# Kernel tuning notes

Measured on AMD Instinct MI355X. Metric: run time of the kernel, lower is better.

## Reference

```python
import jax, jax.numpy as jnp
import numpy as np

N_NODES = 10000
N_EDGES = 100000
IN_CH = 384
PROJ = 768  # in_channels * projection_factor
N_BLOCKS = 4
OUT_CH = 128
LN_EPS = 1e-5


def _p(key, shape, fan_in):
    return jax.random.normal(key, shape, dtype=jnp.float32) * (1.0 / np.sqrt(fan_in))


def setup_inputs() -> dict:
    key = jax.random.key(0)
    ks = iter(jax.random.split(key, 64))
    x = jax.random.normal(next(ks), (N_NODES, IN_CH), dtype=jnp.float32)
    edge_index = jax.random.randint(next(ks), (2, N_EDGES), 0, N_NODES, dtype=jnp.int64)
    inp = {
        'x': x,
        'edge_index': edge_index,
        'proj_W': _p(next(ks), (PROJ, IN_CH), IN_CH),
        'proj_b': jnp.zeros((PROJ,), jnp.float32),
        'norm_w': jnp.ones((N_BLOCKS, PROJ), jnp.float32),
        'norm_b': jnp.zeros((N_BLOCKS, PROJ), jnp.float32),
        'g1_W': _p(next(ks), (N_BLOCKS, 4 * 192, PROJ), PROJ),
        'g1_as': _p(next(ks), (N_BLOCKS, 4, 192), 192),
        'g1_ad': _p(next(ks), (N_BLOCKS, 4, 192), 192),
        'g1_b': jnp.zeros((N_BLOCKS, 4 * 192), jnp.float32),
        'g2_W': _p(next(ks), (N_BLOCKS, 2 * 96, PROJ), PROJ),
        'g2_as': _p(next(ks), (N_BLOCKS, 2, 96), 96),
        'g2_ad': _p(next(ks), (N_BLOCKS, 2, 96), 96),
        'g2_b': jnp.zeros((N_BLOCKS, 2 * 96), jnp.float32),
        'uni_W': _p(next(ks), (N_BLOCKS, PROJ, 960), 960),
        'uni_b': jnp.zeros((N_BLOCKS, PROJ), jnp.float32),
        'fnorm_w': jnp.ones((PROJ,), jnp.float32),
        'fnorm_b': jnp.zeros((PROJ,), jnp.float32),
        'fg_W': _p(next(ks), (8 * OUT_CH, PROJ), PROJ),
        'fg_as': _p(next(ks), (8, OUT_CH), OUT_CH),
        'fg_ad': _p(next(ks), (8, OUT_CH), OUT_CH),
        'fg_b': jnp.zeros((OUT_CH,), jnp.float32),
    }
    return inp


def layer_norm(x, w, b):
    m = x.mean(-1, keepdims=True)
    v = ((x - m) ** 2).mean(-1, keepdims=True)
    return (x - m) / jnp.sqrt(v + LN_EPS) * w + b


def gat_conv(x, src, dst, W, a_src, a_dst, bias, heads, out_ch, concat):
    # PyG GATConv (eval mode, add_self_loops already applied in src/dst).
    n = x.shape[0]
    h = (x @ W.T).reshape(n, heads, out_ch)          # [N,H,C]
    al_s = jnp.einsum('nhc,hc->nh', h, a_src)        # [N,H]
    al_d = jnp.einsum('nhc,hc->nh', h, a_dst)
    e = jax.nn.leaky_relu(al_s[src] + al_d[dst], 0.2)  # [E,H]
    emax = jax.ops.segment_max(e, dst, num_segments=n)
    ee = jnp.exp(e - emax[dst])
    den = jax.ops.segment_sum(ee, dst, num_segments=n)
    alpha = ee / (den[dst] + 1e-16)                  # softmax over incoming edges
    out = jax.ops.segment_sum(h[src] * alpha[:, :, None], dst, num_segments=n)
    out = out.reshape(n, heads * out_ch) if concat else out.mean(axis=1)
    return out + bias


def reference(x, edge_index, proj_W, proj_b, norm_w, norm_b,
              g1_W, g1_as, g1_ad, g1_b, g2_W, g2_as, g2_ad, g2_b,
              uni_W, uni_b, fnorm_w, fnorm_b, fg_W, fg_as, fg_ad, fg_b):
    n = x.shape[0]
    loop = jnp.arange(n, dtype=edge_index.dtype)
    src = jnp.concatenate([edge_index[0], loop])  # add self loops (PyG default)
    dst = jnp.concatenate([edge_index[1], loop])

    h = jax.nn.elu(x @ proj_W.T + proj_b)
    for i in range(N_BLOCKS):
        res = h
        hn = layer_norm(h, norm_w[i], norm_b[i])
        o1 = gat_conv(hn, src, dst, g1_W[i], g1_as[i], g1_ad[i], g1_b[i], 4, 192, True)
        o2 = gat_conv(hn, src, dst, g2_W[i], g2_as[i], g2_ad[i], g2_b[i], 2, 96, True)
        cat = jax.nn.elu(jnp.concatenate([o1, o2], axis=-1))  # [N,960]
        h = jax.nn.elu(res + cat @ uni_W[i].T + uni_b[i])
    h = layer_norm(h, fnorm_w, fnorm_b)
    return gat_conv(h, src, dst, fg_W, fg_as, fg_ad, fg_b, 8, OUT_CH, False)
```

## Files before the change

### kernel.cpp

```cpp
#include <hip/hip_runtime.h>
#include <math.h>

#define N_NODES 10000
#define N_EDGES 100000
#define E_TOT   (N_EDGES + N_NODES)
#define PROJ    768
#define LN_EPS  1e-5f

typedef __attribute__((ext_vector_type(8))) short bf16x8;
typedef __attribute__((ext_vector_type(4))) short bf16x4;
typedef __attribute__((ext_vector_type(4))) float f32x4;

__device__ __forceinline__ float elu_f(float x){ return x > 0.f ? x : __expf(x) - 1.f; }
__device__ __forceinline__ float bf2f(unsigned short u){ return __uint_as_float(((unsigned int)u) << 16); }
__device__ __forceinline__ unsigned short f2bf(float f){
  unsigned int u = __float_as_uint(f);
  return (unsigned short)((u + 0x7FFFu + ((u >> 16) & 1u)) >> 16);
}

#define GLOAD16(gp, lp) __builtin_amdgcn_global_load_lds((const __attribute__((address_space(1))) void*)(gp), (__attribute__((address_space(3))) void*)(lp), 16, 0, 0)

__global__ void k_count(const int* __restrict__ ei, int* __restrict__ cnt){
  int e = blockIdx.x*blockDim.x + threadIdx.x;
  if (e >= E_TOT) return;
  int dst = (e < N_EDGES) ? ei[N_EDGES + e] : (e - N_EDGES);
  atomicAdd(&cnt[dst], 1);
}

__global__ void k_scan(const int* __restrict__ cnt, int* __restrict__ indptr){
  __shared__ int s[1024];
  __shared__ int s_running;
  int t = threadIdx.x;
  if (t == 0) s_running = 0;
  __syncthreads();
  for (int base = 0; base < N_NODES; base += 1024){
    int v = (base + t < N_NODES) ? cnt[base + t] : 0;
    s[t] = v; __syncthreads();
    for (int off = 1; off < 1024; off <<= 1){
      int add = (t >= off) ? s[t - off] : 0;
      __syncthreads();
      s[t] += add;
      __syncthreads();
    }
    int total = s[1023];
    int run = s_running;
    if (base + t < N_NODES) indptr[base + t] = run + s[t] - v;
    __syncthreads();
    if (t == 0) s_running = run + total;
    __syncthreads();
  }
  if (t == 0) indptr[N_NODES] = s_running;
}

__global__ void k_copy_int(const int* __restrict__ src, int* __restrict__ dst, int n){
  int i = blockIdx.x*blockDim.x + threadIdx.x;
  if (i < n) dst[i] = src[i];
}

__global__ void k_fill(const int* __restrict__ ei, int* __restrict__ pos,
                       int* __restrict__ csr_src, int* __restrict__ csr_dst){
  int e = blockIdx.x*blockDim.x + threadIdx.x;
  if (e >= E_TOT) return;
  int s, d;
  if (e < N_EDGES){ s = ei[e]; d = ei[N_EDGES + e]; }
  else            { s = d = e - N_EDGES; }
  int p = atomicAdd(&pos[d], 1);
  csr_src[p] = s;
  csr_dst[p] = d;
}

__global__ void k_f2bf_arr4(const float4* __restrict__ in, ushort4* __restrict__ out, int n4){
  int i = blockIdx.x*blockDim.x + threadIdx.x;
  if (i < n4){
    float4 v = in[i];
    ushort4 o;
    o.x = f2bf(v.x); o.y = f2bf(v.y); o.z = f2bf(v.z); o.w = f2bf(v.w);
    out[i] = o;
  }
}

__global__ void k_pack_l1l2(const float* __restrict__ g1, const float* __restrict__ g2,
                            unsigned short* __restrict__ dst){
  int i = blockIdx.x*blockDim.x + threadIdx.x;
  if (i >= 737280) return;
  int layer = i / 184320;
  int off4  = i - layer*184320;
  float4 v;
  if (off4 < 147456) v = *((const float4*)(g1 + (size_t)layer*589824) + off4);
  else               v = *((const float4*)(g2 + (size_t)layer*147456) + (off4 - 147456));
  ushort4 o;
  o.x = f2bf(v.x); o.y = f2bf(v.y); o.z = f2bf(v.z); o.w = f2bf(v.w);
  ((ushort4*)(dst + (size_t)layer*737280))[off4] = o;
}

__global__ void k_layernorm_bf(const unsigned short* __restrict__ x, const float* __restrict__ w,
                               const float* __restrict__ b, unsigned short* __restrict__ y){
  int n = blockIdx.x;
  int t = threadIdx.x;
  const unsigned short* xr = x + (size_t)n*PROJ;
  float v0=0.f, v1=0.f, v2=0.f, v3=0.f;
  if (t < 192){
    bf16x4 hv = *(const bf16x4*)(xr + t*4);
    v0 = bf2f((unsigned short)hv.x); v1 = bf2f((unsigned short)hv.y);
    v2 = bf2f((unsigned short)hv.z); v3 = bf2f((unsigned short)hv.w);
  }
  float s  = v0+v1+v2+v3;
  float s2 = v0*v0 + v1*v1 + v2*v2 + v3*v3;
  #pragma unroll
  for (int off = 32; off; off >>= 1){ s += __shfl_down(s, off); s2 += __shfl_down(s2, off); }
  __shared__ float rs[4], rs2[4];
  __shared__ float s_mean, s_rstd;
  int wid = t >> 6, lane = t & 63;
  if (lane == 0){ rs[wid] = s; rs2[wid] = s2; }
  __syncthreads();
  if (t == 0){
    float S  = rs[0]+rs[1]+rs[2]+rs[3];
    float S2 = rs2[0]+rs2[1]+rs2[2]+rs2[3];
    float m  = S * (1.f/768.f);
    float var = S2 * (1.f/768.f) - m*m;
    s_mean = m; s_rstd = rsqrtf(var + LN_EPS);
  }
  __syncthreads();
  if (t < 192){
    float m = s_mean, r = s_rstd;
    float4 wv = *(const float4*)&w[t*4];
    float4 bv = *(const float4*)&b[t*4];
    ushort4 o;
    o.x = f2bf((v0-m)*r*wv.x + bv.x);
    o.y = f2bf((v1-m)*r*wv.y + bv.y);
    o.z = f2bf((v2-m)*r*wv.z + bv.z);
    o.w = f2bf((v3-m)*r*wv.w + bv.w);
    *(ushort4*)(y + (size_t)n*PROJ + t*4) = o;
  }
}

template<int EPI>
__global__ __launch_bounds__(256, 8)
void k_gemm_mfma(const unsigned short* __restrict__ A, int lda,
                 const unsigned short* __restrict__ W,
                 unsigned short* __restrict__ C, int ldc,
                 int M, int N, int K,
                 const float* __restrict__ bias,
                 const unsigned short* __restrict__ res, int ldres, int NBN){
  __shared__ unsigned short As[2][128*32];
  __shared__ unsigned short Bs[2][64*32];
  const int tid = threadIdx.x;
  const int lane = tid & 63, wid = tid >> 6;
  const int wm = wid >> 1, wn = wid & 1;

  const int nwg = gridDim.x;
  const int q = nwg >> 3, r = nwg & 7;
  const int xcd = blockIdx.x & 7, o = blockIdx.x >> 3;
  const int swz = (xcd < r ? xcd*(q+1) : r*(q+1) + (xcd - r)*q) + o;
  const int bm = (swz / NBN) * 128;
  const int bn = (swz % NBN) * 64;

  const int srow = tid >> 2;
  const int sc   = (tid & 3) ^ ((tid >> 3) & 3);
  size_t ga0 = (size_t)min(bm + srow,      M-1)*lda + sc*8;
  size_t ga1 = (size_t)min(bm + 64 + srow, M-1)*lda + sc*8;
  size_t gb0 = (size_t)min(bn + srow,      N-1)*K   + sc*8;
  const int ldst = tid*8;

  f32x4 acc[4][2];
  #pragma unroll
  for (int i=0;i<4;i++)
    #pragma unroll
    for (int j=0;j<2;j++) acc[i][j] = (f32x4){0.f,0.f,0.f,0.f};

  const int rA = wm*64 + (lane & 15);
  const int rB = wn*32 + (lane & 15);
  const int cu = (((lane >> 4)) ^ (((lane & 15) >> 1) & 3)) * 8;

  const int NT = K >> 5;
  int cur = 0;
  GLOAD16(A + ga0, &As[0][ldst]);
  GLOAD16(A + ga1, &As[0][2048 + ldst]);
  GLOAD16(W + gb0, &Bs[0][ldst]);

  for (int t = 0; t < NT; ++t){
    if (t + 1 < NT){
      const int k0 = (t+1) << 5;
      GLOAD16(A + ga0 + k0, &As[cur^1][ldst]);
      GLOAD16(A + ga1 + k0, &As[cur^1][2048 + ldst]);
      GLOAD16(W + gb0 + k0, &Bs[cur^1][ldst]);
      asm volatile("s_waitcnt vmcnt(3)" ::: "memory");
    } else {
      asm volatile("s_waitcnt vmcnt(0)" ::: "memory");
    }
    __builtin_amdgcn_sched_barrier(0);
    __builtin_amdgcn_s_barrier();
    __builtin_amdgcn_sched_barrier(0);

    bf16x8 af[4], bfr[2];
    #pragma unroll
    for (int mi = 0; mi < 4; mi++)
      af[mi] = *(const bf16x8*)&As[cur][(rA + mi*16)*32 + cu];
    #pragma unroll
    for (int ni = 0; ni < 2; ni++)
      bfr[ni] = *(const bf16x8*)&Bs[cur][(rB + ni*16)*32 + cu];
    #pragma unroll
    for (int mi = 0; mi < 4; mi++)
      #pragma unroll
      for (int ni = 0; ni < 2; ni++)
        acc[mi][ni] = __builtin_amdgcn_mfma_f32_16x16x32_bf16(af[mi], bfr[ni], acc[mi][ni], 0,0,0);

    asm volatile("s_waitcnt lgkmcnt(0)" ::: "memory");
    __builtin_amdgcn_sched_barrier(0);
    __builtin_amdgcn_s_barrier();
    __builtin_amdgcn_sched_barrier(0);
    cur ^= 1;
  }

  const int mrow0 = bm + wm*64 + ((lane>>4)<<2);
  const int ncol0 = bn + wn*32 + (lane & 15);
  #pragma unroll
  for (int mi=0; mi<4; mi++){
    #pragma unroll
    for (int rr=0; rr<4; rr++){
      int m = mrow0 + mi*16 + rr;
      if (m >= M) continue;
      #pragma unroll
      for (int ni=0; ni<2; ni++){
        int n = ncol0 + ni*16;
        float v = acc[mi][ni][rr];
        if (EPI == 1){
          v = elu_f(v + bias[n]);
        } else if (EPI == 2){
          v = elu_f(v + bias[n] + bf2f(res[(size_t)m*ldres + n]));
        }
        C[(size_t)m*ldc + n] = f2bf(v);
      }
    }
  }
}

__global__ void k_attn_coef6(const unsigned short* __restrict__ hlin,
                             const float* __restrict__ as1, const float* __restrict__ ad1,
                             const float* __restrict__ as2, const float* __restrict__ ad2,
                             float* __restrict__ als, float* __restrict__ ald){
  int n = blockIdx.x;
  int wid = threadIdx.x >> 6, lane = threadIdx.x & 63;
  int C    = wid < 4 ? 192 : 96;
  int base = wid < 4 ? wid*192 : 768 + (wid-4)*96;
  const float* as_ = wid < 4 ? as1 + wid*192 : as2 + (wid-4)*96;
  const float* ad_ = wid < 4 ? ad1 + wid*192 : ad2 + (wid-4)*96;
  float ss = 0.f, sd = 0.f;
  if (lane*4 < C){
    bf16x4 hv = *(const bf16x4*)(hlin + (size_t)n*960 + base + lane*4);
    float4 a1 = *(const float4*)&as_[lane*4];
    float4 a2 = *(const float4*)&ad_[lane*4];
    float h0 = bf2f((unsigned short)hv.x), h1 = bf2f((unsigned short)hv.y);
    float h2 = bf2f((unsigned short)hv.z), h3 = bf2f((unsigned short)hv.w);
    ss = h0*a1.x + h1*a1.y + h2*a1.z + h3*a1.w;
    sd = h0*a2.x + h1*a2.y + h2*a2.z + h3*a2.w;
  }
  #pragma unroll
  for (int off = 32; off; off >>= 1){ ss += __shfl_down(ss, off); sd += __shfl_down(sd, off); }
  if (lane == 0){ als[n*6 + wid] = ss; ald[n*6 + wid] = sd; }
}

__global__ void k_attn_coef8(const unsigned short* __restrict__ hlin,
                             const float* __restrict__ a_src, const float* __restrict__ a_dst,
                             float* __restrict__ als, float* __restrict__ ald){
  int n = blockIdx.x;
  int wid = threadIdx.x >> 6, lane = threadIdx.x & 63;
  float ss = 0.f, sd = 0.f;
  if (lane < 32){
    bf16x4 hv = *(const bf16x4*)(hlin + (size_t)n*1024 + wid*128 + lane*4);
    float4 a1 = *(const float4*)&a_src[wid*128 + lane*4];
    float4 a2 = *(const float4*)&a_dst[wid*128 + lane*4];
    float h0 = bf2f((unsigned short)hv.x), h1 = bf2f((unsigned short)hv.y);
    float h2 = bf2f((unsigned short)hv.z), h3 = bf2f((unsigned short)hv.w);
    ss = h0*a1.x + h1*a1.y + h2*a1.z + h3*a1.w;
    sd = h0*a2.x + h1*a2.y + h2*a2.z + h3*a2.w;
  }
  #pragma unroll
  for (int off = 32; off; off >>= 1){ ss += __shfl_down(ss, off); sd += __shfl_down(sd, off); }
  if (lane == 0){ als[n*8 + wid] = ss; ald[n*8 + wid] = sd; }
}

template<int HT>
__global__ void k_attn_stats(const float* __restrict__ als, const float* __restrict__ ald,
                             const int* __restrict__ indptr, const int* __restrict__ csr_src,
                             float* __restrict__ mo, float* __restrict__ dio){
  int n = blockIdx.x;
  int wv = threadIdx.x >> 6, lane = threadIdx.x & 63;
  int beg = indptr[n], end = indptr[n+1];
  float aldv = ald[n*HT + wv];
  float m = -1e30f, d = 0.f;
  for (int e = beg + lane; e < end; e += 64){
    int s = csr_src[e];
    float v = als[s*HT + wv] + aldv;
    v = v > 0.f ? v : 0.2f*v;
    if (v > m){ d *= __expf(m - v); m = v; }
    d += __expf(v - m);
  }
  #pragma unroll
  for (int off = 1; off < 64; off <<= 1){
    float mo_ = __shfl_xor(m, off);
    float dd  = __shfl_xor(d, off);
    float mn  = fmaxf(m, mo_);
    d = d*__expf(m - mn) + dd*__expf(mo_ - mn);
    m = mn;
  }
  if (lane == 0){ mo[n*HT + wv] = m; dio[n*HT + wv] = 1.f/(d + 1e-16f); }
}

template<int HT>
__global__ void k_attn_alpha(const float* __restrict__ als, const float* __restrict__ ald,
                             const int* __restrict__ csr_src, const int* __restrict__ csr_dst,
                             const float* __restrict__ m, const float* __restrict__ dinv,
                             float* __restrict__ alpha){
  int i = blockIdx.x*blockDim.x + threadIdx.x;
  if (i >= E_TOT*HT) return;
  int e = i / HT, h = i - e*HT;
  int s = csr_src[e], d = csr_dst[e];
  float v = als[s*HT + h] + ald[d*HT + h];
  v = v > 0.f ? v : 0.2f*v;
  alpha[i] = __expf(v - m[d*HT + h]) * dinv[d*HT + h];
}

template<int MODE>
__global__ __launch_bounds__(256)
void k_attn_agg2(const unsigned short* __restrict__ hlin, int ldh,
                 const float* __restrict__ alpha,
                 const int* __restrict__ indptr, const int* __restrict__ csr_src,
                 const float* __restrict__ b1, const float* __restrict__ b2,
                 void* __restrict__ outv, int ldo){
  constexpr int TOT = MODE ? 1024 : 960;
  constexpr int HT  = MODE ? 8 : 6;
  constexpr int CH8 = TOT/8;
  constexpr int CPL = (CH8 + 63)/64;
  int n = blockIdx.x;
  int tid = threadIdx.x;
  int wv = tid >> 6, lane = tid & 63;
  int beg = indptr[n], end = indptr[n+1];

  __shared__ float s_red[4][TOT];

  int hof[CPL];
  #pragma unroll
  for (int p = 0; p < CPL; p++){
    int idx = (lane + p*64)*8;
    hof[p] = MODE ? (idx >> 7) : (idx < 768 ? idx/192 : 4 + (idx-768)/96);
  }

  f32x4 accA[CPL], accB[CPL];
  #pragma unroll
  for (int p = 0; p < CPL; p++){ accA[p] = (f32x4){0,0,0,0}; accB[p] = (f32x4){0,0,0,0}; }

  for (int e = beg + wv; e < end; e += 4){
    int s = csr_src[e];
    const bf16x8* hr = (const bf16x8*)(hlin + (size_t)s*ldh);
    const float* ae = alpha + (size_t)e*HT;
    #pragma unroll
    for (int p = 0; p < CPL; p++){
      int ch = lane + p*64;
      if (CH8 % 64 == 0 || ch < CH8){
        float al = ae[hof[p]];
        bf16x8 hv = hr[ch];
        accA[p].x += bf2f((unsigned short)hv[0])*al;
        accA[p].y += bf2f((unsigned short)hv[1])*al;
        accA[p].z += bf2f((unsigned short)hv[2])*al;
        accA[p].w += bf2f((unsigned short)hv[3])*al;
        accB[p].x += bf2f((unsigned short)hv[4])*al;
        accB[p].y += bf2f((unsigned short)hv[5])*al;
        accB[p].z += bf2f((unsigned short)hv[6])*al;
        accB[p].w += bf2f((unsigned short)hv[7])*al;
      }
    }
  }

  #pragma unroll
  for (int p = 0; p < CPL; p++){
    int ch = lane + p*64;
    if (CH8 % 64 == 0 || ch < CH8){
      *(f32x4*)&s_red[wv][ch*8]     = accA[p];
      *(f32x4*)&s_red[wv][ch*8 + 4] = accB[p];
    }
  }
  __syncthreads();

  if (MODE == 0){
    unsigned short* out = (unsigned short*)outv;
    #pragma unroll
    for (int qq = 0; qq < 4; qq++){
      int idx = tid + qq*256;
      if (idx < TOT){
        float bb = idx < 768 ? b1[idx] : b2[idx - 768];
        float v = s_red[0][idx] + s_red[1][idx] + s_red[2][idx] + s_red[3][idx] + bb;
        out[(size_t)n*ldo + idx] = f2bf(elu_f(v));
      }
    }
  } else {
    float* out = (float*)outv;
    if (tid < 128){
      float v = 0.f;
      #pragma unroll
      for (int h = 0; h < 8; h++){
        int idx = h*128 + tid;
        v += s_red[0][idx] + s_red[1][idx] + s_red[2][idx] + s_red[3][idx];
      }
      out[(size_t)n*ldo + tid] = v*0.125f + b1[tid];
    }
  }
}

extern "C" void kernel_launch(void* const* d_in, const int* in_sizes, int n_in,
                              void* d_out, int out_size, void* d_ws, size_t ws_size,
                              hipStream_t stream){
  const float* x      = (const float*)d_in[0];
  const int*   ei     = (const int*)  d_in[1];
  const float* proj_W = (const float*)d_in[2];
  const float* proj_b = (const float*)d_in[3];
  const float* norm_w = (const float*)d_in[4];
  const float* norm_b = (const float*)d_in[5];
  const float* g1_W   = (const float*)d_in[6];
  const float* g1_as  = (const float*)d_in[7];
  const float* g1_ad  = (const float*)d_in[8];
  const float* g1_b   = (const float*)d_in[9];
  const float* g2_W   = (const float*)d_in[10];
  const float* g2_as  = (const float*)d_in[11];
  const float* g2_ad  = (const float*)d_in[12];
  const float* g2_b   = (const float*)d_in[13];
  const float* uni_W  = (const float*)d_in[14];
  const float* uni_b  = (const float*)d_in[15];
  const float* fnorm_w= (const float*)d_in[16];
  const float* fnorm_b= (const float*)d_in[17];
  const float* fg_W   = (const float*)d_in[18];
  const float* fg_as  = (const float*)d_in[19];
  const float* fg_ad  = (const float*)d_in[20];
  const float* fg_b   = (const float*)d_in[21];

  float* w = (float*)d_ws;
  unsigned short* h  = (unsigned short*)w; w += 3840000;
  unsigned short* h2 = (unsigned short*)w; w += 3840000;
  unsigned short* linbuf = (unsigned short*)w; w += 5120000;
  unsigned short* hnb  = (unsigned short*)w; w += 3840000;
  unsigned short* catb = (unsigned short*)w; w += 4800000;
  unsigned short* wb   = (unsigned short*)w; w += 3489792;
  float* als   = w; w += 80000;
  float* ald   = w; w += 80000;
  float* mbuf  = w; w += 80000;
  float* dibuf = w; w += 80000;
  float* alphab= w; w += 880000;
  int* iw = (int*)w;
  int* cnt     = iw; iw += 10016;
  int* indptr  = iw; iw += 10016;
  int* pos     = iw; iw += 10016;
  int* csr_src = iw; iw += 110016;
  int* csr_dst = iw; iw += 110016;

  unsigned short* wb_proj = wb;
  unsigned short* wb_l12  = wb_proj + 294912;
  unsigned short* wb_uni  = wb_l12 + 2949120;
  unsigned short* wb_fg   = wb_uni + 2949120;

  hipMemsetAsync(cnt, 0, N_NODES*sizeof(int), stream);
  k_count<<<(E_TOT+255)/256, 256, 0, stream>>>(ei, cnt);
  k_scan<<<1, 1024, 0, stream>>>(cnt, indptr);
  k_copy_int<<<(N_NODES+255)/256, 256, 0, stream>>>(indptr, pos, N_NODES);
  k_fill<<<(E_TOT+255)/256, 256, 0, stream>>>(ei, pos, csr_src, csr_dst);

  k_f2bf_arr4<<<(960000+255)/256, 256, 0, stream>>>((const float4*)x, (ushort4*)hnb, 960000);
  k_f2bf_arr4<<<(73728+255)/256,  256, 0, stream>>>((const float4*)proj_W, (ushort4*)wb_proj, 73728);
  k_pack_l1l2<<<(737280+255)/256, 256, 0, stream>>>(g1_W, g2_W, wb_l12);
  k_f2bf_arr4<<<(737280+255)/256, 256, 0, stream>>>((const float4*)uni_W, (ushort4*)wb_uni, 737280);
  k_f2bf_arr4<<<(196608+255)/256, 256, 0, stream>>>((const float4*)fg_W, (ushort4*)wb_fg, 196608);

  dim3 blk(256);

  k_gemm_mfma<1><<<dim3(79*12), blk, 0, stream>>>(hnb, 384, wb_proj, h, 768, N_NODES, 768, 384, proj_b, nullptr, 0, 12);

  unsigned short* cur = h;
  unsigned short* oth = h2;
  for (int i = 0; i < 4; i++){
    k_layernorm_bf<<<N_NODES, 256, 0, stream>>>(cur, norm_w + i*768, norm_b + i*768, hnb);
    k_gemm_mfma<0><<<dim3(79*15), blk, 0, stream>>>(hnb, 768, wb_l12 + (size_t)i*737280, linbuf, 960, N_NODES, 960, 768, nullptr, nullptr, 0, 15);
    k_attn_coef6<<<N_NODES, 384, 0, stream>>>(linbuf, g1_as + i*768, g1_ad + i*768, g2_as + i*192, g2_ad + i*192, als, ald);
    k_attn_stats<6><<<N_NODES, 384, 0, stream>>>(als, ald, indptr, csr_src, mbuf, dibuf);
    k_attn_alpha<6><<<(E_TOT*6+255)/256, 256, 0, stream>>>(als, ald, csr_src, csr_dst, mbuf, dibuf, alphab);
    k_attn_agg2<0><<<N_NODES, 256, 0, stream>>>(linbuf, 960, alphab, indptr, csr_src, g1_b + i*768, g2_b + i*192, catb, 960);
    k_gemm_mfma<2><<<dim3(79*12), blk, 0, stream>>>(catb, 960, wb_uni + (size_t)i*737280, oth, 768, N_NODES, 768, 960, uni_b + i*768, cur, 768, 12);
    unsigned short* t = cur; cur = oth; oth = t;
  }

  k_layernorm_bf<<<N_NODES, 256, 0, stream>>>(cur, fnorm_w, fnorm_b, hnb);
  k_gemm_mfma<0><<<dim3(79*16), blk, 0, stream>>>(hnb, 768, wb_fg, linbuf, 1024, N_NODES, 1024, 768, nullptr, nullptr, 0, 16);
  k_attn_coef8<<<N_NODES, 512, 0, stream>>>(linbuf, fg_as, fg_ad, als, ald);
  k_attn_stats<8><<<N_NODES, 512, 0, stream>>>(als, ald, indptr, csr_src, mbuf, dibuf);
  k_attn_alpha<8><<<(E_TOT*8+255)/256, 256, 0, stream>>>(als, ald, csr_src, csr_dst, mbuf, dibuf, alphab);
  k_attn_agg2<1><<<N_NODES, 256, 0, stream>>>(linbuf, 1024, alphab, indptr, csr_src, fg_b, nullptr, d_out, 128);
}
```

Measured before the change: 765.2 us.

## Switch MFMA GEMM to single-wave 64x64 tiles without workgroup barriers

The bf16 MFMA GEMM drops from a 4-wave workgroup computing a 128x64 tile to a single 64-lane wave computing a 64x64 tile, and the grids grow accordingly. Each wave now stages its own A and B tiles through double-buffered LDS with direct global-to-LDS loads. Because only one wave shares the tile, both s_barrier synchronisations per k-step go away, and each wave does more MFMAs per loaded fragment. The cost is less data reuse across waves within a workgroup, so more global/L2 traffic per output element, plus more register pressure from the 4x4 accumulator set.

```diff
diff --git a/kernel.cpp b/kernel.cpp
--- a/kernel.cpp
+++ b/kernel.cpp
@@ -135,85 +135,81 @@
 }
 
 template<int EPI>
-__global__ __launch_bounds__(256, 8)
+__global__ __launch_bounds__(64, 4)
 void k_gemm_mfma(const unsigned short* __restrict__ A, int lda,
                  const unsigned short* __restrict__ W,
                  unsigned short* __restrict__ C, int ldc,
                  int M, int N, int K,
                  const float* __restrict__ bias,
                  const unsigned short* __restrict__ res, int ldres, int NBN){
-  __shared__ unsigned short As[2][128*32];
-  __shared__ unsigned short Bs[2][64*32];
-  const int tid = threadIdx.x;
-  const int lane = tid & 63, wid = tid >> 6;
-  const int wm = wid >> 1, wn = wid & 1;
+  __shared__ unsigned short Aw[2][64*32];
+  __shared__ unsigned short Bw[2][64*32];
+  const int lane = threadIdx.x;
 
   const int nwg = gridDim.x;
   const int q = nwg >> 3, r = nwg & 7;
   const int xcd = blockIdx.x & 7, o = blockIdx.x >> 3;
   const int swz = (xcd < r ? xcd*(q+1) : r*(q+1) + (xcd - r)*q) + o;
-  const int bm = (swz / NBN) * 128;
+  const int bm = (swz / NBN) * 64;
   const int bn = (swz % NBN) * 64;
 
-  const int srow = tid >> 2;
-  const int sc   = (tid & 3) ^ ((tid >> 3) & 3);
-  size_t ga0 = (size_t)min(bm + srow,      M-1)*lda + sc*8;
-  size_t ga1 = (size_t)min(bm + 64 + srow, M-1)*lda + sc*8;
-  size_t gb0 = (size_t)min(bn + srow,      N-1)*K   + sc*8;
-  const int ldst = tid*8;
-
-  f32x4 acc[4][2];
+  const int sc = (lane & 3) ^ ((lane >> 3) & 3);
+  size_t ga[4], gb[4];
+  #pragma unroll
+  for (int p = 0; p < 4; p++){
+    ga[p] = (size_t)min(bm + p*16 + (lane>>2), M-1)*lda + sc*8;
+    gb[p] = (size_t)min(bn + p*16 + (lane>>2), N-1)*K   + sc*8;
+  }
+  const int ldst = lane*8;
+
+  f32x4 acc[4][4];
   #pragma unroll
   for (int i=0;i<4;i++)
     #pragma unroll
-    for (int j=0;j<2;j++) acc[i][j] = (f32x4){0.f,0.f,0.f,0.f};
-
-  const int rA = wm*64 + (lane & 15);
-  const int rB = wn*32 + (lane & 15);
-  const int cu = (((lane >> 4)) ^ (((lane & 15) >> 1) & 3)) * 8;
+    for (int j=0;j<4;j++) acc[i][j] = (f32x4){0.f,0.f,0.f,0.f};
+
+  const int cu = ((lane >> 4) ^ (((lane & 15) >> 1) & 3)) * 8;
+  const int rr0 = lane & 15;
 
   const int NT = K >> 5;
   int cur = 0;
-  GLOAD16(A + ga0, &As[0][ldst]);
-  GLOAD16(A + ga1, &As[0][2048 + ldst]);
-  GLOAD16(W + gb0, &Bs[0][ldst]);
+  #pragma unroll
+  for (int p = 0; p < 4; p++){
+    GLOAD16(A + ga[p], &Aw[0][p*512 + ldst]);
+    GLOAD16(W + gb[p], &Bw[0][p*512 + ldst]);
+  }
 
   for (int t = 0; t < NT; ++t){
     if (t + 1 < NT){
       const int k0 = (t+1) << 5;
-      GLOAD16(A + ga0 + k0, &As[cur^1][ldst]);
-      GLOAD16(A + ga1 + k0, &As[cur^1][2048 + ldst]);
-      GLOAD16(W + gb0 + k0, &Bs[cur^1][ldst]);
-      asm volatile("s_waitcnt vmcnt(3)" ::: "memory");
+      #pragma unroll
+      for (int p = 0; p < 4; p++){
+        GLOAD16(A + ga[p] + k0, &Aw[cur^1][p*512 + ldst]);
+        GLOAD16(W + gb[p] + k0, &Bw[cur^1][p*512 + ldst]);
+      }
+      asm volatile("s_waitcnt vmcnt(8)" ::: "memory");
     } else {
       asm volatile("s_waitcnt vmcnt(0)" ::: "memory");
     }
     __builtin_amdgcn_sched_barrier(0);
-    __builtin_amdgcn_s_barrier();
-    __builtin_amdgcn_sched_barrier(0);
-
-    bf16x8 af[4], bfr[2];
+
+    bf16x8 af[4], bfr[4];
     #pragma unroll
     for (int mi = 0; mi < 4; mi++)
-      af[mi] = *(const bf16x8*)&As[cur][(rA + mi*16)*32 + cu];
-    #pragma unroll
-    for (int ni = 0; ni < 2; ni++)
-      bfr[ni] = *(const bf16x8*)&Bs[cur][(rB + ni*16)*32 + cu];
+      af[mi] = *(const bf16x8*)&Aw[cur][(rr0 + mi*16)*32 + cu];
+    #pragma unroll
+    for (int ni = 0; ni < 4; ni++)
+      bfr[ni] = *(const bf16x8*)&Bw[cur][(rr0 + ni*16)*32 + cu];
     #pragma unroll
     for (int mi = 0; mi < 4; mi++)
       #pragma unroll
-      for (int ni = 0; ni < 2; ni++)
+      for (int ni = 0; ni < 4; ni++)
         acc[mi][ni] = __builtin_amdgcn_mfma_f32_16x16x32_bf16(af[mi], bfr[ni], acc[mi][ni], 0,0,0);
-
-    asm volatile("s_waitcnt lgkmcnt(0)" ::: "memory");
-    __builtin_amdgcn_sched_barrier(0);
-    __builtin_amdgcn_s_barrier();
-    __builtin_amdgcn_sched_barrier(0);
     cur ^= 1;
   }
 
-  const int mrow0 = bm + wm*64 + ((lane>>4)<<2);
-  const int ncol0 = bn + wn*32 + (lane & 15);
+  const int mrow0 = bm + ((lane>>4)<<2);
+  const int ncol0 = bn + (lane & 15);
   #pragma unroll
   for (int mi=0; mi<4; mi++){
     #pragma unroll
@@ -221,7 +217,7 @@
       int m = mrow0 + mi*16 + rr;
       if (m >= M) continue;
       #pragma unroll
-      for (int ni=0; ni<2; ni++){
+      for (int ni=0; ni<4; ni++){
         int n = ncol0 + ni*16;
         float v = acc[mi][ni][rr];
         if (EPI == 1){
@@ -470,24 +466,26 @@
   k_f2bf_arr4<<<(196608+255)/256, 256, 0, stream>>>((const float4*)fg_W, (ushort4*)wb_fg, 196608);
 
   dim3 blk(256);
-
-  k_gemm_mfma<1><<<dim3(79*12), blk, 0, stream>>>(hnb, 384, wb_proj, h, 768, N_NODES, 768, 384, proj_b, nullptr, 0, 12);
+  dim3 gblk(64);
+  const int GM = 157;
+
+  k_gemm_mfma<1><<<dim3(GM*12), gblk, 0, stream>>>(hnb, 384, wb_proj, h, 768, N_NODES, 768, 384, proj_b, nullptr, 0, 12);
 
   unsigned short* cur = h;
   unsigned short* oth = h2;
   for (int i = 0; i < 4; i++){
     k_layernorm_bf<<<N_NODES, 256, 0, stream>>>(cur, norm_w + i*768, norm_b + i*768, hnb);
-    k_gemm_mfma<0><<<dim3(79*15), blk, 0, stream>>>(hnb, 768, wb_l12 + (size_t)i*737280, linbuf, 960, N_NODES, 960, 768, nullptr, nullptr, 0, 15);
+    k_gemm_mfma<0><<<dim3(GM*15), gblk, 0, stream>>>(hnb, 768, wb_l12 + (size_t)i*737280, linbuf, 960, N_NODES, 960, 768, nullptr, nullptr, 0, 15);
     k_attn_coef6<<<N_NODES, 384, 0, stream>>>(linbuf, g1_as + i*768, g1_ad + i*768, g2_as + i*192, g2_ad + i*192, als, ald);
     k_attn_stats<6><<<N_NODES, 384, 0, stream>>>(als, ald, indptr, csr_src, mbuf, dibuf);
     k_attn_alpha<6><<<(E_TOT*6+255)/256, 256, 0, stream>>>(als, ald, csr_src, csr_dst, mbuf, dibuf, alphab);
     k_attn_agg2<0><<<N_NODES, 256, 0, stream>>>(linbuf, 960, alphab, indptr, csr_src, g1_b + i*768, g2_b + i*192, catb, 960);
-    k_gemm_mfma<2><<<dim3(79*12), blk, 0, stream>>>(catb, 960, wb_uni + (size_t)i*737280, oth, 768, N_NODES, 768, 960, uni_b + i*768, cur, 768, 12);
+    k_gemm_mfma<2><<<dim3(GM*12), gblk, 0, stream>>>(catb, 960, wb_uni + (size_t)i*737280, oth, 768, N_NODES, 768, 960, uni_b + i*768, cur, 768, 12);
     unsigned short* t = cur; cur = oth; oth = t;
   }
 
   k_layernorm_bf<<<N_NODES, 256, 0, stream>>>(cur, fnorm_w, fnorm_b, hnb);
-  k_gemm_mfma<0><<<dim3(79*16), blk, 0, stream>>>(hnb, 768, wb_fg, linbuf, 1024, N_NODES, 1024, 768, nullptr, nullptr, 0, 16);
+  k_gemm_mfma<0><<<dim3(GM*16), gblk, 0, stream>>>(hnb, 768, wb_fg, linbuf, 1024, N_NODES, 1024, 768, nullptr, nullptr, 0, 16);
   k_attn_coef8<<<N_NODES, 512, 0, stream>>>(linbuf, fg_as, fg_ad, als, ald);
   k_attn_stats<8><<<N_NODES, 512, 0, stream>>>(als, ald, indptr, csr_src, mbuf, dibuf);
   k_attn_alpha<8><<<(E_TOT*8+255)/256, 256, 0, stream>>>(als, ald, csr_src, csr_dst, mbuf, dibuf, alphab);
```

Result: slower. 865.0 us (+13.0%).

## Fuse GAT softmax stats, alpha and aggregation into one per-node kernel

Applied to the files above, without the earlier changes.

Replaces the separate attention-statistics, per-edge alpha and aggregation kernels with a single per-destination-node kernel. It computes the softmax max and denominator in-block, then builds alpha for chunks of 64 edges in shared memory before accumulating features. The scan now writes the fill cursor directly, which removes the copy kernel and the csr_dst array. This drops launches and global alpha/m/dinv traffic, at the cost of extra block syncs and redundant per-node reductions inside the aggregation kernel.

```diff
diff --git a/kernel.cpp b/kernel.cpp
--- a/kernel.cpp
+++ b/kernel.cpp
@@ -27,7 +27,7 @@
   atomicAdd(&cnt[dst], 1);
 }
 
-__global__ void k_scan(const int* __restrict__ cnt, int* __restrict__ indptr){
+__global__ void k_scan(const int* __restrict__ cnt, int* __restrict__ indptr, int* __restrict__ pos){
   __shared__ int s[1024];
   __shared__ int s_running;
   int t = threadIdx.x;
@@ -44,7 +44,11 @@
     }
     int total = s[1023];
     int run = s_running;
-    if (base + t < N_NODES) indptr[base + t] = run + s[t] - v;
+    if (base + t < N_NODES){
+      int val = run + s[t] - v;
+      indptr[base + t] = val;
+      pos[base + t] = val;
+    }
     __syncthreads();
     if (t == 0) s_running = run + total;
     __syncthreads();
@@ -52,13 +56,8 @@
   if (t == 0) indptr[N_NODES] = s_running;
 }
 
-__global__ void k_copy_int(const int* __restrict__ src, int* __restrict__ dst, int n){
-  int i = blockIdx.x*blockDim.x + threadIdx.x;
-  if (i < n) dst[i] = src[i];
-}
-
 __global__ void k_fill(const int* __restrict__ ei, int* __restrict__ pos,
-                       int* __restrict__ csr_src, int* __restrict__ csr_dst){
+                       int* __restrict__ csr_src){
   int e = blockIdx.x*blockDim.x + threadIdx.x;
   if (e >= E_TOT) return;
   int s, d;
@@ -66,7 +65,6 @@
   else            { s = d = e - N_EDGES; }
   int p = atomicAdd(&pos[d], 1);
   csr_src[p] = s;
-  csr_dst[p] = d;
 }
 
 __global__ void k_f2bf_arr4(const float4* __restrict__ in, ushort4* __restrict__ out, int n4){
@@ -280,54 +278,13 @@
   if (lane == 0){ als[n*8 + wid] = ss; ald[n*8 + wid] = sd; }
 }
 
-template<int HT>
-__global__ void k_attn_stats(const float* __restrict__ als, const float* __restrict__ ald,
-                             const int* __restrict__ indptr, const int* __restrict__ csr_src,
-                             float* __restrict__ mo, float* __restrict__ dio){
-  int n = blockIdx.x;
-  int wv = threadIdx.x >> 6, lane = threadIdx.x & 63;
-  int beg = indptr[n], end = indptr[n+1];
-  float aldv = ald[n*HT + wv];
-  float m = -1e30f, d = 0.f;
-  for (int e = beg + lane; e < end; e += 64){
-    int s = csr_src[e];
-    float v = als[s*HT + wv] + aldv;
-    v = v > 0.f ? v : 0.2f*v;
-    if (v > m){ d *= __expf(m - v); m = v; }
-    d += __expf(v - m);
-  }
-  #pragma unroll
-  for (int off = 1; off < 64; off <<= 1){
-    float mo_ = __shfl_xor(m, off);
-    float dd  = __shfl_xor(d, off);
-    float mn  = fmaxf(m, mo_);
-    d = d*__expf(m - mn) + dd*__expf(mo_ - mn);
-    m = mn;
-  }
-  if (lane == 0){ mo[n*HT + wv] = m; dio[n*HT + wv] = 1.f/(d + 1e-16f); }
-}
-
-template<int HT>
-__global__ void k_attn_alpha(const float* __restrict__ als, const float* __restrict__ ald,
-                             const int* __restrict__ csr_src, const int* __restrict__ csr_dst,
-                             const float* __restrict__ m, const float* __restrict__ dinv,
-                             float* __restrict__ alpha){
-  int i = blockIdx.x*blockDim.x + threadIdx.x;
-  if (i >= E_TOT*HT) return;
-  int e = i / HT, h = i - e*HT;
-  int s = csr_src[e], d = csr_dst[e];
-  float v = als[s*HT + h] + ald[d*HT + h];
-  v = v > 0.f ? v : 0.2f*v;
-  alpha[i] = __expf(v - m[d*HT + h]) * dinv[d*HT + h];
-}
-
 template<int MODE>
 __global__ __launch_bounds__(256)
-void k_attn_agg2(const unsigned short* __restrict__ hlin, int ldh,
-                 const float* __restrict__ alpha,
-                 const int* __restrict__ indptr, const int* __restrict__ csr_src,
-                 const float* __restrict__ b1, const float* __restrict__ b2,
-                 void* __restrict__ outv, int ldo){
+void k_attn_fused(const unsigned short* __restrict__ hlin, int ldh,
+                  const float* __restrict__ als, const float* __restrict__ ald,
+                  const int* __restrict__ indptr, const int* __restrict__ csr_src,
+                  const float* __restrict__ b1, const float* __restrict__ b2,
+                  void* __restrict__ outv, int ldo){
   constexpr int TOT = MODE ? 1024 : 960;
   constexpr int HT  = MODE ? 8 : 6;
   constexpr int CH8 = TOT/8;
@@ -335,9 +292,33 @@
   int n = blockIdx.x;
   int tid = threadIdx.x;
   int wv = tid >> 6, lane = tid & 63;
-  int beg = indptr[n], end = indptr[n+1];
-
+  int beg = indptr[n], end = indptr[n+1], deg = end - beg;
+
+  __shared__ float s_m[HT], s_dinv[HT], s_ald[HT];
+  __shared__ float s_alpha[64*HT];
+  __shared__ int   s_src[64];
   __shared__ float s_red[4][TOT];
+
+  for (int h = wv; h < HT; h += 4){
+    float aldv = ald[n*HT + h];
+    float m = -1e30f, d = 0.f;
+    for (int e = beg + lane; e < end; e += 64){
+      int s = csr_src[e];
+      float v = als[s*HT + h] + aldv;
+      v = v > 0.f ? v : 0.2f*v;
+      if (v > m){ d *= __expf(m - v); m = v; }
+      d += __expf(v - m);
+    }
+    #pragma unroll
+    for (int off = 1; off < 64; off <<= 1){
+      float mo_ = __shfl_xor(m, off);
+      float dd  = __shfl_xor(d, off);
+      float mn  = fmaxf(m, mo_);
+      d = d*__expf(m - mn) + dd*__expf(mo_ - mn);
+      m = mn;
+    }
+    if (lane == 0){ s_m[h] = m; s_dinv[h] = 1.f/(d + 1e-16f); s_ald[h] = aldv; }
+  }
 
   int hof[CPL];
   #pragma unroll
@@ -350,24 +331,37 @@
   #pragma unroll
   for (int p = 0; p < CPL; p++){ accA[p] = (f32x4){0,0,0,0}; accB[p] = (f32x4){0,0,0,0}; }
 
-  for (int e = beg + wv; e < end; e += 4){
-    int s = csr_src[e];
-    const bf16x8* hr = (const bf16x8*)(hlin + (size_t)s*ldh);
-    const float* ae = alpha + (size_t)e*HT;
-    #pragma unroll
-    for (int p = 0; p < CPL; p++){
-      int ch = lane + p*64;
-      if (CH8 % 64 == 0 || ch < CH8){
-        float al = ae[hof[p]];
-        bf16x8 hv = hr[ch];
-        accA[p].x += bf2f((unsigned short)hv[0])*al;
-        accA[p].y += bf2f((unsigned short)hv[1])*al;
-        accA[p].z += bf2f((unsigned short)hv[2])*al;
-        accA[p].w += bf2f((unsigned short)hv[3])*al;
-        accB[p].x += bf2f((unsigned short)hv[4])*al;
-        accB[p].y += bf2f((unsigned short)hv[5])*al;
-        accB[p].z += bf2f((unsigned short)hv[6])*al;
-        accB[p].w += bf2f((unsigned short)hv[7])*al;
+  for (int base = 0; base < deg; base += 64){
+    int chunk = min(64, deg - base);
+    __syncthreads();
+    if (tid < chunk) s_src[tid] = csr_src[beg + base + tid];
+    __syncthreads();
+    for (int i = tid; i < chunk*HT; i += 256){
+      int e = i / HT, h = i - e*HT;
+      float v = als[s_src[e]*HT + h] + s_ald[h];
+      v = v > 0.f ? v : 0.2f*v;
+      s_alpha[e*HT + h] = __expf(v - s_m[h]) * s_dinv[h];
+    }
+    __syncthreads();
+    for (int e = wv; e < chunk; e += 4){
+      int s = s_src[e];
+      const bf16x8* hr = (const bf16x8*)(hlin + (size_t)s*ldh);
+      const float* ae = &s_alpha[e*HT];
+      #pragma unroll
+      for (int p = 0; p < CPL; p++){
+        int ch = lane + p*64;
+        if (CH8 % 64 == 0 || ch < CH8){
+          float al = ae[hof[p]];
+          bf16x8 hv = hr[ch];
+          accA[p].x += bf2f((unsigned short)hv[0])*al;
+          accA[p].y += bf2f((unsigned short)hv[1])*al;
+          accA[p].z += bf2f((unsigned short)hv[2])*al;
+          accA[p].w += bf2f((unsigned short)hv[3])*al;
+          accB[p].x += bf2f((unsigned short)hv[4])*al;
+          accB[p].y += bf2f((unsigned short)hv[5])*al;
+          accB[p].z += bf2f((unsigned short)hv[6])*al;
+          accB[p].w += bf2f((unsigned short)hv[7])*al;
+        }
       }
     }
   }
@@ -442,15 +436,11 @@
   unsigned short* wb   = (unsigned short*)w; w += 3489792;
   float* als   = w; w += 80000;
   float* ald   = w; w += 80000;
-  float* mbuf  = w; w += 80000;
-  float* dibuf = w; w += 80000;
-  float* alphab= w; w += 880000;
   int* iw = (int*)w;
   int* cnt     = iw; iw += 10016;
   int* indptr  = iw; iw += 10016;
   int* pos     = iw; iw += 10016;
   int* csr_src = iw; iw += 110016;
-  int* csr_dst = iw; iw += 110016;
 
   unsigned short* wb_proj = wb;
   unsigned short* wb_l12  = wb_proj + 294912;
@@ -459,9 +449,8 @@
 
   hipMemsetAsync(cnt, 0, N_NODES*sizeof(int), stream);
   k_count<<<(E_TOT+255)/256, 256, 0, stream>>>(ei, cnt);
-  k_scan<<<1, 1024, 0, stream>>>(cnt, indptr);
-  k_copy_int<<<(N_NODES+255)/256, 256, 0, stream>>>(indptr, pos, N_NODES);
-  k_fill<<<(E_TOT+255)/256, 256, 0, stream>>>(ei, pos, csr_src, csr_dst);
+  k_scan<<<1, 1024, 0, stream>>>(cnt, indptr, pos);
+  k_fill<<<(E_TOT+255)/256, 256, 0, stream>>>(ei, pos, csr_src);
 
   k_f2bf_arr4<<<(960000+255)/256, 256, 0, stream>>>((const float4*)x, (ushort4*)hnb, 960000);
   k_f2bf_arr4<<<(73728+255)/256,  256, 0, stream>>>((const float4*)proj_W, (ushort4*)wb_proj, 73728);
@@ -479,9 +468,7 @@
     k_layernorm_bf<<<N_NODES, 256, 0, stream>>>(cur, norm_w + i*768, norm_b + i*768, hnb);
     k_gemm_mfma<0><<<dim3(79*15), blk, 0, stream>>>(hnb, 768, wb_l12 + (size_t)i*737280, linbuf, 960, N_NODES, 960, 768, nullptr, nullptr, 0, 15);
     k_attn_coef6<<<N_NODES, 384, 0, stream>>>(linbuf, g1_as + i*768, g1_ad + i*768, g2_as + i*192, g2_ad + i*192, als, ald);
-    k_attn_stats<6><<<N_NODES, 384, 0, stream>>>(als, ald, indptr, csr_src, mbuf, dibuf);
-    k_attn_alpha<6><<<(E_TOT*6+255)/256, 256, 0, stream>>>(als, ald, csr_src, csr_dst, mbuf, dibuf, alphab);
-    k_attn_agg2<0><<<N_NODES, 256, 0, stream>>>(linbuf, 960, alphab, indptr, csr_src, g1_b + i*768, g2_b + i*192, catb, 960);
+    k_attn_fused<0><<<N_NODES, 256, 0, stream>>>(linbuf, 960, als, ald, indptr, csr_src, g1_b + i*768, g2_b + i*192, catb, 960);
     k_gemm_mfma<2><<<dim3(79*12), blk, 0, stream>>>(catb, 960, wb_uni + (size_t)i*737280, oth, 768, N_NODES, 768, 960, uni_b + i*768, cur, 768, 12);
     unsigned short* t = cur; cur = oth; oth = t;
   }
@@ -489,7 +476,5 @@
   k_layernorm_bf<<<N_NODES, 256, 0, stream>>>(cur, fnorm_w, fnorm_b, hnb);
   k_gemm_mfma<0><<<dim3(79*16), blk, 0, stream>>>(hnb, 768, wb_fg, linbuf, 1024, N_NODES, 1024, 768, nullptr, nullptr, 0, 16);
   k_attn_coef8<<<N_NODES, 512, 0, stream>>>(linbuf, fg_as, fg_ad, als, ald);
-  k_attn_stats<8><<<N_NODES, 512, 0, stream>>>(als, ald, indptr, csr_src, mbuf, dibuf);
-  k_attn_alpha<8><<<(E_TOT*8+255)/256, 256, 0, stream>>>(als, ald, csr_src, csr_dst, mbuf, dibuf, alphab);
-  k_attn_agg2<1><<<N_NODES, 256, 0, stream>>>(linbuf, 1024, alphab, indptr, csr_src, fg_b, nullptr, d_out, 128);
-}
+  k_attn_fused<1><<<N_NODES, 256, 0, stream>>>(linbuf, 1024, als, ald, indptr, csr_src, fg_b, nullptr, d_out, 128);
+}
```

New measurement: 696.4 us. 9.0% less time.
